# Optimization experiments

Hardware: AMD Instinct MI355X
Metric: run time of the kernel (lower is better)

The kernel has to match this reference:

```python
import jax, jax.numpy as jnp
import numpy as np

EMBED_DIM = 1024
NUM_HEADS = 16
HEAD_DIM = EMBED_DIM // NUM_HEADS
BATCH = 4
SEQ = 2048


def setup_inputs() -> dict:
    key = jax.random.key(0)
    ks = jax.random.split(key, 9)
    s = 1.0 / np.sqrt(EMBED_DIM)
    return {
        "query": jax.random.normal(ks[0], (BATCH, SEQ, EMBED_DIM), jnp.float32),
        "Wq": jax.random.normal(ks[1], (EMBED_DIM, EMBED_DIM), jnp.float32) * s,
        "bq": jnp.zeros((EMBED_DIM,), jnp.float32),
        "Wk": jax.random.normal(ks[2], (EMBED_DIM, EMBED_DIM), jnp.float32) * s,
        "bk": jnp.zeros((EMBED_DIM,), jnp.float32),
        "Wv": jax.random.normal(ks[3], (EMBED_DIM, EMBED_DIM), jnp.float32) * s,
        "bv": jnp.zeros((EMBED_DIM,), jnp.float32),
        "Wo": jax.random.normal(ks[4], (EMBED_DIM, EMBED_DIM), jnp.float32) * s,
        "bo": jnp.zeros((EMBED_DIM,), jnp.float32),
    }


def reference(query, Wq, bq, Wk, bk, Wv, bv, Wo, bo):
    bsz, seq, embed_dim = query.shape
    scaling = HEAD_DIM ** (-0.5)
    # projections (torch Linear: x @ W.T + b)
    q = (query @ Wq.T + bq) * scaling
    k = query @ Wk.T + bk
    v = query @ Wv.T + bv
    # [b, h, s, d]
    q = q.reshape(bsz, seq, NUM_HEADS, HEAD_DIM).transpose(0, 2, 1, 3)
    k = k.reshape(bsz, seq, NUM_HEADS, HEAD_DIM).transpose(0, 2, 1, 3)
    v = v.reshape(bsz, seq, NUM_HEADS, HEAD_DIM).transpose(0, 2, 1, 3)
    # full [b, h, s, s] scores (faithful to the naive original)
    scores = jnp.einsum("bhqd,bhkd->bhqk", q, k)
    causal = jnp.tril(jnp.ones((seq, seq), bool))  # [s, s]
    scores = jnp.where(causal[None, None], scores, -jnp.inf)
    probs = jax.nn.softmax(scores, axis=-1)
    attn = jnp.einsum("bhqk,bhkd->bhqd", probs, v)
    attn = attn.transpose(0, 2, 1, 3).reshape(bsz, seq, embed_dim)
    return attn @ Wo.T + bo
```

## Files before the change

kernel.cpp:

```cpp
#include <hip/hip_runtime.h>
#include <stdint.h>

typedef unsigned short u16;
typedef __attribute__((ext_vector_type(8))) __bf16 bf16x8;
typedef __attribute__((ext_vector_type(4))) float f32x4;

#define SEQL 2048
#define NHEADS 16
#define HDIM 64
#define BSZ 4
#define EMB 1024
#define MROWS (BSZ * SEQL)
#define LOG2E 1.44269504088896f
#define NKT 32

__device__ __forceinline__ u16 f2bf(float f) {
  union { float f; uint32_t u; } v; v.f = f;
  return (u16)((v.u + 0x7fffu + ((v.u >> 16) & 1u)) >> 16);
}

__device__ __forceinline__ void g2l(const u16* g, u16* l) {
  __builtin_amdgcn_global_load_lds(
      (__attribute__((address_space(1))) void*)(g),
      (__attribute__((address_space(3))) void*)(l), 16, 0, 0);
}

__device__ __forceinline__ void cvt8(const float* __restrict__ in, u16* __restrict__ out, int i) {
  float4 a = *(const float4*)(in + i);
  float4 b = *(const float4*)(in + i + 4);
  uint4 o;
  o.x = f2bf(a.x) | ((uint32_t)f2bf(a.y) << 16);
  o.y = f2bf(a.z) | ((uint32_t)f2bf(a.w) << 16);
  o.z = f2bf(b.x) | ((uint32_t)f2bf(b.y) << 16);
  o.w = f2bf(b.z) | ((uint32_t)f2bf(b.w) << 16);
  *(uint4*)(out + i) = o;
}

#define XN (MROWS * EMB)
__global__ void cvt_all(const float* __restrict__ query,
                        const float* __restrict__ w0, const float* __restrict__ w1,
                        const float* __restrict__ w2, const float* __restrict__ w3,
                        u16* __restrict__ Xb, u16* __restrict__ Wqb) {
  int i = (blockIdx.x * blockDim.x + threadIdx.x) * 8;
  if (i < XN) {
    cvt8(query, Xb, i);
  } else {
    int j = i - XN;
    int w = j >> 20;
    int jj = j & 1048575;
    const float* src = w == 0 ? w0 : w == 1 ? w1 : w == 2 ? w2 : w3;
    cvt8(src, Wqb + ((size_t)w << 20), jj);
  }
}

#define GBODY3(WSTR, RBUF, DOPF, PFT, WBUF)                                         \
  {                                                                                 \
    asm volatile("s_waitcnt " WSTR ::: "memory");                                   \
    __builtin_amdgcn_sched_barrier(0);                                              \
    __builtin_amdgcn_s_barrier();                                                   \
    __builtin_amdgcn_sched_barrier(0);                                              \
    if (DOPF) {                                                                     \
      u16* d = lds + (WBUF) * 12288;                                                \
      g2l(Agb + (PFT) * 32, d + tid * 8);                                           \
      g2l(Bgb0 + (PFT) * 32, d + 4096 + tid * 8);                                   \
      g2l(Bgb1 + (PFT) * 32, d + 8192 + tid * 8);                                   \
    }                                                                               \
    const u16* Ab = lds + (RBUF) * 12288;                                           \
    const u16* Bb = Ab + 4096;                                                      \
    bf16x8 af[4], bfr[4];                                                           \
    _Pragma("unroll") for (int i = 0; i < 4; ++i) {                                 \
      af[i] = *(const bf16x8*)(Ab + (wr * 64 + i * 16 + lrow) * 32 + kg);           \
      bfr[i] = *(const bf16x8*)(Bb + (wc * 64 + i * 16 + lrow) * 32 + kg);          \
    }                                                                               \
    __builtin_amdgcn_s_setprio(1);                                                  \
    _Pragma("unroll") for (int mi = 0; mi < 4; ++mi)                                \
      _Pragma("unroll") for (int ni = 0; ni < 4; ++ni)                              \
        acc[mi][ni] =                                                               \
            __builtin_amdgcn_mfma_f32_16x16x32_bf16(af[mi], bfr[ni], acc[mi][ni],   \
                                                    0, 0, 0);                       \
    __builtin_amdgcn_s_setprio(0);                                                  \
  }

__device__ __forceinline__ void gemm_core256(const u16* __restrict__ A,
                                             const u16* __restrict__ B,
                                             int m0, int n0, u16* lds,
                                             f32x4 acc[4][4]) {
  const int tid = threadIdx.x;
  const int lane = tid & 63, wid = tid >> 6;
  const int wr = wid >> 2, wc = wid & 3;
  const int lrow = lane & 15, kg = (lane >> 4) * 8;
  const int srow = tid >> 2, scolE = (tid & 3) * 8;

  const u16* Agb  = A + (size_t)(m0 + srow) * EMB + scolE;
  const u16* Bgb0 = B + (size_t)(n0 + srow) * EMB + scolE;
  const u16* Bgb1 = B + (size_t)(n0 + 128 + srow) * EMB + scolE;

#pragma unroll
  for (int t = 0; t < 2; ++t) {
    u16* d = lds + t * 12288;
    g2l(Agb + t * 32, d + tid * 8);
    g2l(Bgb0 + t * 32, d + 4096 + tid * 8);
    g2l(Bgb1 + t * 32, d + 8192 + tid * 8);
  }

  int rb = 0;
#pragma unroll 1
  for (int kt = 0; kt < NKT - 2; ++kt) {
    int wb = rb + 2; if (wb >= 3) wb -= 3;
    GBODY3("vmcnt(3)", rb, true, kt + 2, wb)
    ++rb; if (rb == 3) rb = 0;
  }
  GBODY3("vmcnt(3)", rb, false, 0, 0)
  { int rb2 = rb + 1; if (rb2 == 3) rb2 = 0;
    GBODY3("vmcnt(0)", rb2, false, 0, 0) }
}

__global__ __launch_bounds__(512, 4) void gemm_qkv3(
    const u16* __restrict__ X, const u16* __restrict__ Wcat,
    const float* __restrict__ bq, const float* __restrict__ bk, const float* __restrict__ bv,
    u16* __restrict__ Qb, u16* __restrict__ Kb, u16* __restrict__ Vt) {
  __shared__ u16 lds[3 * 12288];
  const int orig = blockIdx.x;
  const int virt = (orig & 7) * 96 + (orig >> 3);
  const int mt = virt / 12, nt = virt % 12;

  const f32x4 fzero = {0.f, 0.f, 0.f, 0.f};
  f32x4 acc[4][4];
#pragma unroll
  for (int i = 0; i < 4; ++i)
#pragma unroll
    for (int j = 0; j < 4; ++j) acc[i][j] = fzero;

  gemm_core256(X, Wcat, mt * 128, nt * 256, lds, acc);

  const int tid = threadIdx.x, lane = tid & 63, wid = tid >> 6;
  const int wr = wid >> 2, wc = wid & 3;
  const int lrow = lane & 15, g = lane >> 4;
  const int which = nt >> 2;
  const float* bias = which == 0 ? bq : which == 1 ? bk : bv;
  const float scale = which == 0 ? 0.125f * LOG2E : 1.0f;

  if (which == 2) {
#pragma unroll
    for (int mi = 0; mi < 4; ++mi)
#pragma unroll
      for (int ni = 0; ni < 4; ++ni) {
        int n = nt * 256 + wc * 64 + ni * 16 + lrow;
        int nn = n & 1023;
        float bs = bias[nn];
        int h = nn >> 6, d = nn & 63;
        int m0r = mt * 128 + wr * 64 + mi * 16 + g * 4;
        int b = m0r >> 11, s = m0r & 2047;
        union { u16 s4[4]; uint2 u; } o;
#pragma unroll
        for (int r = 0; r < 4; ++r) o.s4[r] = f2bf(acc[mi][ni][r] + bs);
        *(uint2*)(Vt + ((size_t)(b * NHEADS + h) * HDIM + d) * SEQL + s) = o.u;
      }
  } else {
    u16* Ob = which == 0 ? Qb : Kb;
#pragma unroll
    for (int mi = 0; mi < 4; ++mi)
#pragma unroll
      for (int ni = 0; ni < 4; ++ni) {
        int n = nt * 256 + wc * 64 + ni * 16 + lrow;
        int nn = n & 1023;
        float bs = bias[nn];
        int h = nn >> 6, d = nn & 63;
#pragma unroll
        for (int r = 0; r < 4; ++r) {
          int m = mt * 128 + wr * 64 + mi * 16 + g * 4 + r;
          int b = m >> 11, s = m & 2047;
          float v = (acc[mi][ni][r] + bs) * scale;
          Ob[(size_t)((b * NHEADS + h) * SEQL + s) * HDIM + d] = f2bf(v);
        }
      }
  }
}

__global__ __launch_bounds__(512, 4) void gemm_out2(
    const u16* __restrict__ Ain, const u16* __restrict__ Wo,
    const float* __restrict__ bo, float* __restrict__ out) {
  __shared__ u16 lds[3 * 12288];
  const int orig = blockIdx.x;
  const int virt = (orig & 7) * 32 + (orig >> 3);
  const int mt = virt >> 2, nt = virt & 3;

  const f32x4 fzero = {0.f, 0.f, 0.f, 0.f};
  f32x4 acc[4][4];
#pragma unroll
  for (int i = 0; i < 4; ++i)
#pragma unroll
    for (int j = 0; j < 4; ++j) acc[i][j] = fzero;

  gemm_core256(Ain, Wo, mt * 128, nt * 256, lds, acc);

  const int tid = threadIdx.x, lane = tid & 63, wid = tid >> 6;
  const int wr = wid >> 2, wc = wid & 3;
  const int lrow = lane & 15, g = lane >> 4;
#pragma unroll
  for (int mi = 0; mi < 4; ++mi)
#pragma unroll
    for (int ni = 0; ni < 4; ++ni) {
      int n = nt * 256 + wc * 64 + ni * 16 + lrow;
      float bs = bo[n];
#pragma unroll
      for (int r = 0; r < 4; ++r) {
        int m = mt * 128 + wr * 64 + mi * 16 + g * 4 + r;
        out[(size_t)m * EMB + n] = acc[mi][ni][r] + bs;
      }
    }
}

__device__ __forceinline__ int swz(int row, int colE) {
  return row * 64 + (colE ^ ((row & 7) << 3));
}

__global__ __launch_bounds__(256, 4) void attn4_kernel(
    const u16* __restrict__ Qb, const u16* __restrict__ Kb, const u16* __restrict__ Vt,
    u16* __restrict__ Ab) {
  __shared__ u16 Ks[2][64 * 64];
  __shared__ u16 Vs[2][64 * 64];

  const int bid = blockIdx.x;
  const int qa  = bid >> 6;
  const int bh  = bid & 63;

  const int tid = threadIdx.x, lane = tid & 63, wid = tid >> 6;
  const int lrow = lane & 15, g = lane >> 4, kg = g * 8;

  const u16* Qbh = Qb + (size_t)bh * SEQL * HDIM;
  const u16* Kbh = Kb + (size_t)bh * SEQL * HDIM;
  const u16* Vbh = Vt + (size_t)bh * HDIM * SEQL;

  const int srow = tid >> 3;
  const int sce  = (tid & 7) * 8;

  const f32x4 fzero = {0.f, 0.f, 0.f, 0.f};
  const int b = bh >> 4, h = bh & 15;

#pragma unroll 1
  for (int ph = 0; ph < 2; ++ph) {
    const int qt = ph ? (31 - qa) : qa;
    const int q0 = qt * 64;
    const int NT = qt + 1;

    const int qrow = q0 + wid * 16 + lrow;
    const bf16x8 qf0 = *(const bf16x8*)(Qbh + (size_t)qrow * HDIM + kg);
    const bf16x8 qf1 = *(const bf16x8*)(Qbh + (size_t)qrow * HDIM + 32 + kg);

    float m_run = -1e30f, l_run = 0.f;
    f32x4 accO[4];
#pragma unroll
    for (int d = 0; d < 4; ++d) accO[d] = fzero;

    {
      uint4 k0 = *(const uint4*)(Kbh + (size_t)srow * HDIM + sce);
      uint4 k1 = *(const uint4*)(Kbh + (size_t)(srow + 32) * HDIM + sce);
      uint4 v0 = *(const uint4*)(Vbh + (size_t)srow * SEQL + sce);
      uint4 v1 = *(const uint4*)(Vbh + (size_t)(srow + 32) * SEQL + sce);
      *(uint4*)(&Ks[0][swz(srow, sce)]) = k0;
      *(uint4*)(&Ks[0][swz(srow + 32, sce)]) = k1;
      *(uint4*)(&Vs[0][swz(srow, sce)]) = v0;
      *(uint4*)(&Vs[0][swz(srow + 32, sce)]) = v1;
    }
    __syncthreads();

    for (int t = 0; t < NT; ++t) {
      const int cur = t & 1;
      const int kv0 = t * 64;
      const bool pf = (t + 1 < NT);
      uint4 k0, k1, v0, v1;
      if (pf) {
        const int kvn = kv0 + 64;
        k0 = *(const uint4*)(Kbh + (size_t)(kvn + srow) * HDIM + sce);
        k1 = *(const uint4*)(Kbh + (size_t)(kvn + srow + 32) * HDIM + sce);
        v0 = *(const uint4*)(Vbh + (size_t)srow * SEQL + kvn + sce);
        v1 = *(const uint4*)(Vbh + (size_t)(srow + 32) * SEQL + kvn + sce);
      }

      f32x4 sacc[4];
      __builtin_amdgcn_s_setprio(1);
#pragma unroll
      for (int kb = 0; kb < 4; ++kb) {
        bf16x8 kfa = *(const bf16x8*)(&Ks[cur][swz(kb * 16 + lrow, kg)]);
        bf16x8 kfb = *(const bf16x8*)(&Ks[cur][swz(kb * 16 + lrow, 32 + kg)]);
        f32x4 z = fzero;
        z = __builtin_amdgcn_mfma_f32_16x16x32_bf16(kfa, qf0, z, 0, 0, 0);
        z = __builtin_amdgcn_mfma_f32_16x16x32_bf16(kfb, qf1, z, 0, 0, 0);
        sacc[kb] = z;
      }
      __builtin_amdgcn_s_setprio(0);

      if (kv0 + 63 > q0 + wid * 16) {
#pragma unroll
        for (int kb = 0; kb < 4; ++kb)
#pragma unroll
          for (int r = 0; r < 4; ++r)
            if (kv0 + kb * 16 + g * 4 + r > qrow) sacc[kb][r] = -1e30f;
      }

      float mx = sacc[0][0];
#pragma unroll
      for (int kb = 0; kb < 4; ++kb)
#pragma unroll
        for (int r = 0; r < 4; ++r) mx = fmaxf(mx, sacc[kb][r]);
      mx = fmaxf(mx, __shfl_xor(mx, 16));
      mx = fmaxf(mx, __shfl_xor(mx, 32));

      if (!__all(mx <= m_run + 8.f)) {
        const float mnew = fmaxf(m_run, mx);
        const float sc = __builtin_amdgcn_exp2f(m_run - mnew);
        m_run = mnew;
        l_run *= sc;
#pragma unroll
        for (int d = 0; d < 4; ++d) accO[d] *= sc;
      }

      bf16x8 pa[2];
      float ls = 0.f;
#pragma unroll
      for (int kb = 0; kb < 4; ++kb)
#pragma unroll
        for (int r = 0; r < 4; ++r) {
          float p = __builtin_amdgcn_exp2f(sacc[kb][r] - m_run);
          ls += p;
          pa[kb >> 1][(kb & 1) * 4 + r] = (__bf16)p;
        }
      l_run += ls;

      __builtin_amdgcn_s_setprio(1);
#pragma unroll
      for (int ks = 0; ks < 2; ++ks)
#pragma unroll
        for (int d = 0; d < 4; ++d) {
          union { ushort4 h2[2]; bf16x8 v; } vf;
          vf.h2[0] = *(const ushort4*)(&Vs[cur][swz(d * 16 + lrow, ks * 32 + g * 4)]);
          vf.h2[1] = *(const ushort4*)(&Vs[cur][swz(d * 16 + lrow, ks * 32 + 16 + g * 4)]);
          accO[d] = __builtin_amdgcn_mfma_f32_16x16x32_bf16(vf.v, pa[ks], accO[d], 0, 0, 0);
        }
      __builtin_amdgcn_s_setprio(0);

      if (pf) {
        const int nb = cur ^ 1;
        *(uint4*)(&Ks[nb][swz(srow, sce)]) = k0;
        *(uint4*)(&Ks[nb][swz(srow + 32, sce)]) = k1;
        *(uint4*)(&Vs[nb][swz(srow, sce)]) = v0;
        *(uint4*)(&Vs[nb][swz(srow + 32, sce)]) = v1;
      }
      __syncthreads();
    }

    float l = l_run;
    l += __shfl_xor(l, 16);
    l += __shfl_xor(l, 32);
    const float inv = 1.f / l;
#pragma unroll
    for (int d = 0; d < 4; ++d) {
      union { u16 s4[4]; uint2 u; } o;
#pragma unroll
      for (int r = 0; r < 4; ++r) o.s4[r] = f2bf(accO[d][r] * inv);
      *(uint2*)(Ab + (size_t)(b * SEQL + qrow) * EMB + h * HDIM + d * 16 + g * 4) = o.u;
    }
    __syncthreads();
  }
}

extern "C" void kernel_launch(void* const* d_in, const int* in_sizes, int n_in,
                              void* d_out, int out_size, void* d_ws, size_t ws_size,
                              hipStream_t stream) {
  (void)in_sizes; (void)n_in; (void)out_size; (void)ws_size;
  const float* query = (const float*)d_in[0];
  const float* Wq = (const float*)d_in[1];
  const float* bq = (const float*)d_in[2];
  const float* Wk = (const float*)d_in[3];
  const float* bk = (const float*)d_in[4];
  const float* Wv = (const float*)d_in[5];
  const float* bv = (const float*)d_in[6];
  const float* Wo = (const float*)d_in[7];
  const float* bo = (const float*)d_in[8];
  float* out = (float*)d_out;

  const size_t MB = 1u << 20;
  char* ws = (char*)d_ws;
  u16* Xb  = (u16*)(ws);
  u16* Wqb = (u16*)(ws + 16 * MB);
  u16* Wob = (u16*)(ws + 22 * MB);
  u16* Qbf = (u16*)(ws + 24 * MB);
  u16* Kbf = (u16*)(ws + 40 * MB);
  u16* Vtg = (u16*)(ws + 56 * MB);
  u16* Ab  = Xb;

  cvt_all<<<6144, 256, 0, stream>>>(query, Wq, Wk, Wv, Wo, Xb, Wqb);
  gemm_qkv3<<<768, 512, 0, stream>>>(Xb, Wqb, bq, bk, bv, Qbf, Kbf, Vtg);
  attn4_kernel<<<1024, 256, 0, stream>>>(Qbf, Kbf, Vtg, Ab);
  gemm_out2<<<256, 512, 0, stream>>>(Ab, Wob, bo, out);
}
```

Before: 160.1 us.

## Shrink GEMM tiles to 128x128 with 4-wave blocks; tree-reduce softmax max/sum

Both projection GEMMs move from 128x256 tiles on 8-wave blocks to 128x128 tiles on 4-wave blocks. That doubles the grid (1536 and 512 blocks) and cuts LDS per stage, with matching changes to the staging loads, vmcnt counts, swizzled block mapping and epilogue indexing. The aim is better occupancy and tail balance, especially for the output GEMM, which previously had only 256 blocks. The cost is less operand reuse per block and more global and L2 traffic. The attention kernel also switches its row max and exp-sum to tree reductions to shorten serial dependency chains.

```diff
diff --git a/kernel.cpp b/kernel.cpp
--- a/kernel.cpp
+++ b/kernel.cpp
@@ -53,19 +53,20 @@
   }
 }
 
-#define GBODY3(WSTR, RBUF, DOPF, PFT, WBUF)                                         \
+#define GBODY2(WSTR, RBUF, DOPF, PFT, WBUF)                                         \
   {                                                                                 \
     asm volatile("s_waitcnt " WSTR ::: "memory");                                   \
     __builtin_amdgcn_sched_barrier(0);                                              \
     __builtin_amdgcn_s_barrier();                                                   \
     __builtin_amdgcn_sched_barrier(0);                                              \
     if (DOPF) {                                                                     \
-      u16* d = lds + (WBUF) * 12288;                                                \
+      u16* d = lds + (WBUF) * 8192;                                                 \
       g2l(Agb + (PFT) * 32, d + tid * 8);                                           \
-      g2l(Bgb0 + (PFT) * 32, d + 4096 + tid * 8);                                   \
-      g2l(Bgb1 + (PFT) * 32, d + 8192 + tid * 8);                                   \
+      g2l(Agb + (PFT) * 32 + 64 * EMB, d + 2048 + tid * 8);                         \
+      g2l(Bgb + (PFT) * 32, d + 4096 + tid * 8);                                    \
+      g2l(Bgb + (PFT) * 32 + 64 * EMB, d + 6144 + tid * 8);                         \
     }                                                                               \
-    const u16* Ab = lds + (RBUF) * 12288;                                           \
+    const u16* Ab = lds + (RBUF) * 8192;                                            \
     const u16* Bb = Ab + 4096;                                                      \
     bf16x8 af[4], bfr[4];                                                           \
     _Pragma("unroll") for (int i = 0; i < 4; ++i) {                                 \
@@ -81,48 +82,48 @@
     __builtin_amdgcn_s_setprio(0);                                                  \
   }
 
-__device__ __forceinline__ void gemm_core256(const u16* __restrict__ A,
+__device__ __forceinline__ void gemm_core128(const u16* __restrict__ A,
                                              const u16* __restrict__ B,
                                              int m0, int n0, u16* lds,
                                              f32x4 acc[4][4]) {
   const int tid = threadIdx.x;
   const int lane = tid & 63, wid = tid >> 6;
-  const int wr = wid >> 2, wc = wid & 3;
+  const int wr = wid >> 1, wc = wid & 1;
   const int lrow = lane & 15, kg = (lane >> 4) * 8;
   const int srow = tid >> 2, scolE = (tid & 3) * 8;
 
-  const u16* Agb  = A + (size_t)(m0 + srow) * EMB + scolE;
-  const u16* Bgb0 = B + (size_t)(n0 + srow) * EMB + scolE;
-  const u16* Bgb1 = B + (size_t)(n0 + 128 + srow) * EMB + scolE;
+  const u16* Agb = A + (size_t)(m0 + srow) * EMB + scolE;
+  const u16* Bgb = B + (size_t)(n0 + srow) * EMB + scolE;
 
 #pragma unroll
   for (int t = 0; t < 2; ++t) {
-    u16* d = lds + t * 12288;
+    u16* d = lds + t * 8192;
     g2l(Agb + t * 32, d + tid * 8);
-    g2l(Bgb0 + t * 32, d + 4096 + tid * 8);
-    g2l(Bgb1 + t * 32, d + 8192 + tid * 8);
+    g2l(Agb + t * 32 + 64 * EMB, d + 2048 + tid * 8);
+    g2l(Bgb + t * 32, d + 4096 + tid * 8);
+    g2l(Bgb + t * 32 + 64 * EMB, d + 6144 + tid * 8);
   }
 
   int rb = 0;
 #pragma unroll 1
   for (int kt = 0; kt < NKT - 2; ++kt) {
     int wb = rb + 2; if (wb >= 3) wb -= 3;
-    GBODY3("vmcnt(3)", rb, true, kt + 2, wb)
+    GBODY2("vmcnt(4)", rb, true, kt + 2, wb)
     ++rb; if (rb == 3) rb = 0;
   }
-  GBODY3("vmcnt(3)", rb, false, 0, 0)
+  GBODY2("vmcnt(4)", rb, false, 0, 0)
   { int rb2 = rb + 1; if (rb2 == 3) rb2 = 0;
-    GBODY3("vmcnt(0)", rb2, false, 0, 0) }
-}
-
-__global__ __launch_bounds__(512, 4) void gemm_qkv3(
+    GBODY2("vmcnt(0)", rb2, false, 0, 0) }
+}
+
+__global__ __launch_bounds__(256, 3) void gemm_qkv3(
     const u16* __restrict__ X, const u16* __restrict__ Wcat,
     const float* __restrict__ bq, const float* __restrict__ bk, const float* __restrict__ bv,
     u16* __restrict__ Qb, u16* __restrict__ Kb, u16* __restrict__ Vt) {
-  __shared__ u16 lds[3 * 12288];
+  __shared__ u16 lds[3 * 8192];
   const int orig = blockIdx.x;
-  const int virt = (orig & 7) * 96 + (orig >> 3);
-  const int mt = virt / 12, nt = virt % 12;
+  const int virt = (orig & 7) * 192 + (orig >> 3);
+  const int mt = virt / 24, nt = virt % 24;
 
   const f32x4 fzero = {0.f, 0.f, 0.f, 0.f};
   f32x4 acc[4][4];
@@ -131,12 +132,12 @@
 #pragma unroll
     for (int j = 0; j < 4; ++j) acc[i][j] = fzero;
 
-  gemm_core256(X, Wcat, mt * 128, nt * 256, lds, acc);
+  gemm_core128(X, Wcat, mt * 128, nt * 128, lds, acc);
 
   const int tid = threadIdx.x, lane = tid & 63, wid = tid >> 6;
-  const int wr = wid >> 2, wc = wid & 3;
+  const int wr = wid >> 1, wc = wid & 1;
   const int lrow = lane & 15, g = lane >> 4;
-  const int which = nt >> 2;
+  const int which = nt >> 3;
   const float* bias = which == 0 ? bq : which == 1 ? bk : bv;
   const float scale = which == 0 ? 0.125f * LOG2E : 1.0f;
 
@@ -145,7 +146,7 @@
     for (int mi = 0; mi < 4; ++mi)
 #pragma unroll
       for (int ni = 0; ni < 4; ++ni) {
-        int n = nt * 256 + wc * 64 + ni * 16 + lrow;
+        int n = nt * 128 + wc * 64 + ni * 16 + lrow;
         int nn = n & 1023;
         float bs = bias[nn];
         int h = nn >> 6, d = nn & 63;
@@ -162,7 +163,7 @@
     for (int mi = 0; mi < 4; ++mi)
 #pragma unroll
       for (int ni = 0; ni < 4; ++ni) {
-        int n = nt * 256 + wc * 64 + ni * 16 + lrow;
+        int n = nt * 128 + wc * 64 + ni * 16 + lrow;
         int nn = n & 1023;
         float bs = bias[nn];
         int h = nn >> 6, d = nn & 63;
@@ -177,13 +178,13 @@
   }
 }
 
-__global__ __launch_bounds__(512, 4) void gemm_out2(
+__global__ __launch_bounds__(256, 3) void gemm_out2(
     const u16* __restrict__ Ain, const u16* __restrict__ Wo,
     const float* __restrict__ bo, float* __restrict__ out) {
-  __shared__ u16 lds[3 * 12288];
+  __shared__ u16 lds[3 * 8192];
   const int orig = blockIdx.x;
-  const int virt = (orig & 7) * 32 + (orig >> 3);
-  const int mt = virt >> 2, nt = virt & 3;
+  const int virt = (orig & 7) * 64 + (orig >> 3);
+  const int mt = virt >> 3, nt = virt & 7;
 
   const f32x4 fzero = {0.f, 0.f, 0.f, 0.f};
   f32x4 acc[4][4];
@@ -192,16 +193,16 @@
 #pragma unroll
     for (int j = 0; j < 4; ++j) acc[i][j] = fzero;
 
-  gemm_core256(Ain, Wo, mt * 128, nt * 256, lds, acc);
+  gemm_core128(Ain, Wo, mt * 128, nt * 128, lds, acc);
 
   const int tid = threadIdx.x, lane = tid & 63, wid = tid >> 6;
-  const int wr = wid >> 2, wc = wid & 3;
+  const int wr = wid >> 1, wc = wid & 1;
   const int lrow = lane & 15, g = lane >> 4;
 #pragma unroll
   for (int mi = 0; mi < 4; ++mi)
 #pragma unroll
     for (int ni = 0; ni < 4; ++ni) {
-      int n = nt * 256 + wc * 64 + ni * 16 + lrow;
+      int n = nt * 128 + wc * 64 + ni * 16 + lrow;
       float bs = bo[n];
 #pragma unroll
       for (int r = 0; r < 4; ++r) {
@@ -299,11 +300,11 @@
             if (kv0 + kb * 16 + g * 4 + r > qrow) sacc[kb][r] = -1e30f;
       }
 
-      float mx = sacc[0][0];
-#pragma unroll
-      for (int kb = 0; kb < 4; ++kb)
-#pragma unroll
-        for (int r = 0; r < 4; ++r) mx = fmaxf(mx, sacc[kb][r]);
+      float t0 = fmaxf(fmaxf(sacc[0][0], sacc[0][1]), fmaxf(sacc[0][2], sacc[0][3]));
+      float t1 = fmaxf(fmaxf(sacc[1][0], sacc[1][1]), fmaxf(sacc[1][2], sacc[1][3]));
+      float t2 = fmaxf(fmaxf(sacc[2][0], sacc[2][1]), fmaxf(sacc[2][2], sacc[2][3]));
+      float t3 = fmaxf(fmaxf(sacc[3][0], sacc[3][1]), fmaxf(sacc[3][2], sacc[3][3]));
+      float mx = fmaxf(fmaxf(t0, t1), fmaxf(t2, t3));
       mx = fmaxf(mx, __shfl_xor(mx, 16));
       mx = fmaxf(mx, __shfl_xor(mx, 32));
 
@@ -317,16 +318,20 @@
       }
 
       bf16x8 pa[2];
-      float ls = 0.f;
-#pragma unroll
-      for (int kb = 0; kb < 4; ++kb)
-#pragma unroll
-        for (int r = 0; r < 4; ++r) {
-          float p = __builtin_amdgcn_exp2f(sacc[kb][r] - m_run);
-          ls += p;
-          pa[kb >> 1][(kb & 1) * 4 + r] = (__bf16)p;
-        }
-      l_run += ls;
+      float lp[4];
+#pragma unroll
+      for (int kb = 0; kb < 4; ++kb) {
+        float p0 = __builtin_amdgcn_exp2f(sacc[kb][0] - m_run);
+        float p1 = __builtin_amdgcn_exp2f(sacc[kb][1] - m_run);
+        float p2 = __builtin_amdgcn_exp2f(sacc[kb][2] - m_run);
+        float p3 = __builtin_amdgcn_exp2f(sacc[kb][3] - m_run);
+        lp[kb] = (p0 + p1) + (p2 + p3);
+        pa[kb >> 1][(kb & 1) * 4 + 0] = (__bf16)p0;
+        pa[kb >> 1][(kb & 1) * 4 + 1] = (__bf16)p1;
+        pa[kb >> 1][(kb & 1) * 4 + 2] = (__bf16)p2;
+        pa[kb >> 1][(kb & 1) * 4 + 3] = (__bf16)p3;
+      }
+      l_run += (lp[0] + lp[1]) + (lp[2] + lp[3]);
 
       __builtin_amdgcn_s_setprio(1);
 #pragma unroll
@@ -391,7 +396,7 @@
   u16* Ab  = Xb;
 
   cvt_all<<<6144, 256, 0, stream>>>(query, Wq, Wk, Wv, Wo, Xb, Wqb);
-  gemm_qkv3<<<768, 512, 0, stream>>>(Xb, Wqb, bq, bk, bv, Qbf, Kbf, Vtg);
+  gemm_qkv3<<<1536, 256, 0, stream>>>(Xb, Wqb, bq, bk, bv, Qbf, Kbf, Vtg);
   attn4_kernel<<<1024, 256, 0, stream>>>(Qbf, Kbf, Vtg, Ab);
-  gemm_out2<<<256, 512, 0, stream>>>(Ab, Wob, bo, out);
-}
+  gemm_out2<<<512, 256, 0, stream>>>(Ab, Wob, bo, out);
+}
```

After: 168.9 us. +5.5%, slower.

## Software-pipeline attention: compute next tile's QK scores during current softmax/PV

Applied to the files above, without the earlier changes.

Restructures the attention inner loop so the QK^T MFMAs for tile t+1 are issued in the same iteration as the softmax and PV of tile t. K gets a triple-buffered LDS ring and is prefetched two tiles ahead, while V stays double-buffered one tile ahead. This is meant to let MFMA work overlap the exp/max VALU work and hide LDS latency. In exchange it uses more LDS and registers (sa/sb score sets), which may reduce occupancy, and the loop is now kept rolled with unroll 1.

```diff
diff --git a/kernel.cpp b/kernel.cpp
--- a/kernel.cpp
+++ b/kernel.cpp
@@ -215,10 +215,10 @@
   return row * 64 + (colE ^ ((row & 7) << 3));
 }
 
-__global__ __launch_bounds__(256, 4) void attn4_kernel(
+__global__ __launch_bounds__(256, 4) void attn5_kernel(
     const u16* __restrict__ Qb, const u16* __restrict__ Kb, const u16* __restrict__ Vt,
     u16* __restrict__ Ab) {
-  __shared__ u16 Ks[2][64 * 64];
+  __shared__ u16 Ks[3][64 * 64];
   __shared__ u16 Vs[2][64 * 64];
 
   const int bid = blockIdx.x;
@@ -262,48 +262,80 @@
       *(uint4*)(&Ks[0][swz(srow + 32, sce)]) = k1;
       *(uint4*)(&Vs[0][swz(srow, sce)]) = v0;
       *(uint4*)(&Vs[0][swz(srow + 32, sce)]) = v1;
+      if (NT > 1) {
+        uint4 k2 = *(const uint4*)(Kbh + (size_t)(64 + srow) * HDIM + sce);
+        uint4 k3 = *(const uint4*)(Kbh + (size_t)(64 + srow + 32) * HDIM + sce);
+        *(uint4*)(&Ks[1][swz(srow, sce)]) = k2;
+        *(uint4*)(&Ks[1][swz(srow + 32, sce)]) = k3;
+      }
     }
     __syncthreads();
 
+    f32x4 sa[4];
+    __builtin_amdgcn_s_setprio(1);
+#pragma unroll
+    for (int kb = 0; kb < 4; ++kb) {
+      bf16x8 kfa = *(const bf16x8*)(&Ks[0][swz(kb * 16 + lrow, kg)]);
+      bf16x8 kfb = *(const bf16x8*)(&Ks[0][swz(kb * 16 + lrow, 32 + kg)]);
+      f32x4 z = fzero;
+      z = __builtin_amdgcn_mfma_f32_16x16x32_bf16(kfa, qf0, z, 0, 0, 0);
+      z = __builtin_amdgcn_mfma_f32_16x16x32_bf16(kfb, qf1, z, 0, 0, 0);
+      sa[kb] = z;
+    }
+    __builtin_amdgcn_s_setprio(0);
+    if (63 > q0 + wid * 16) {
+#pragma unroll
+      for (int kb = 0; kb < 4; ++kb)
+#pragma unroll
+        for (int r = 0; r < 4; ++r)
+          if (kb * 16 + g * 4 + r > qrow) sa[kb][r] = -1e30f;
+    }
+
+    int kB1 = 1, kB2 = 2;
+#pragma unroll 1
     for (int t = 0; t < NT; ++t) {
-      const int cur = t & 1;
-      const int kv0 = t * 64;
-      const bool pf = (t + 1 < NT);
-      uint4 k0, k1, v0, v1;
-      if (pf) {
-        const int kvn = kv0 + 64;
-        k0 = *(const uint4*)(Kbh + (size_t)(kvn + srow) * HDIM + sce);
-        k1 = *(const uint4*)(Kbh + (size_t)(kvn + srow + 32) * HDIM + sce);
-        v0 = *(const uint4*)(Vbh + (size_t)srow * SEQL + kvn + sce);
-        v1 = *(const uint4*)(Vbh + (size_t)(srow + 32) * SEQL + kvn + sce);
-      }
-
-      f32x4 sacc[4];
-      __builtin_amdgcn_s_setprio(1);
-#pragma unroll
-      for (int kb = 0; kb < 4; ++kb) {
-        bf16x8 kfa = *(const bf16x8*)(&Ks[cur][swz(kb * 16 + lrow, kg)]);
-        bf16x8 kfb = *(const bf16x8*)(&Ks[cur][swz(kb * 16 + lrow, 32 + kg)]);
-        f32x4 z = fzero;
-        z = __builtin_amdgcn_mfma_f32_16x16x32_bf16(kfa, qf0, z, 0, 0, 0);
-        z = __builtin_amdgcn_mfma_f32_16x16x32_bf16(kfb, qf1, z, 0, 0, 0);
-        sacc[kb] = z;
-      }
-      __builtin_amdgcn_s_setprio(0);
-
-      if (kv0 + 63 > q0 + wid * 16) {
-#pragma unroll
-        for (int kb = 0; kb < 4; ++kb)
-#pragma unroll
-          for (int r = 0; r < 4; ++r)
-            if (kv0 + kb * 16 + g * 4 + r > qrow) sacc[kb][r] = -1e30f;
-      }
-
-      float mx = sacc[0][0];
+      const bool hasN1 = (t + 1 < NT);
+      const bool hasN2 = (t + 2 < NT);
+      uint4 pk0, pk1, pv0, pv1;
+      if (hasN2) {
+        const int kvn = (t + 2) * 64;
+        pk0 = *(const uint4*)(Kbh + (size_t)(kvn + srow) * HDIM + sce);
+        pk1 = *(const uint4*)(Kbh + (size_t)(kvn + srow + 32) * HDIM + sce);
+      }
+      if (hasN1) {
+        const int kvn = (t + 1) * 64;
+        pv0 = *(const uint4*)(Vbh + (size_t)srow * SEQL + kvn + sce);
+        pv1 = *(const uint4*)(Vbh + (size_t)(srow + 32) * SEQL + kvn + sce);
+      }
+
+      f32x4 sb[4];
+      if (hasN1) {
+        __builtin_amdgcn_s_setprio(1);
+#pragma unroll
+        for (int kb = 0; kb < 4; ++kb) {
+          bf16x8 kfa = *(const bf16x8*)(&Ks[kB1][swz(kb * 16 + lrow, kg)]);
+          bf16x8 kfb = *(const bf16x8*)(&Ks[kB1][swz(kb * 16 + lrow, 32 + kg)]);
+          f32x4 z = fzero;
+          z = __builtin_amdgcn_mfma_f32_16x16x32_bf16(kfa, qf0, z, 0, 0, 0);
+          z = __builtin_amdgcn_mfma_f32_16x16x32_bf16(kfb, qf1, z, 0, 0, 0);
+          sb[kb] = z;
+        }
+        __builtin_amdgcn_s_setprio(0);
+        const int kv0n = (t + 1) * 64;
+        if (kv0n + 63 > q0 + wid * 16) {
+#pragma unroll
+          for (int kb = 0; kb < 4; ++kb)
+#pragma unroll
+            for (int r = 0; r < 4; ++r)
+              if (kv0n + kb * 16 + g * 4 + r > qrow) sb[kb][r] = -1e30f;
+        }
+      }
+
+      float mx = sa[0][0];
 #pragma unroll
       for (int kb = 0; kb < 4; ++kb)
 #pragma unroll
-        for (int r = 0; r < 4; ++r) mx = fmaxf(mx, sacc[kb][r]);
+        for (int r = 0; r < 4; ++r) mx = fmaxf(mx, sa[kb][r]);
       mx = fmaxf(mx, __shfl_xor(mx, 16));
       mx = fmaxf(mx, __shfl_xor(mx, 32));
 
@@ -322,7 +354,7 @@
       for (int kb = 0; kb < 4; ++kb)
 #pragma unroll
         for (int r = 0; r < 4; ++r) {
-          float p = __builtin_amdgcn_exp2f(sacc[kb][r] - m_run);
+          float p = __builtin_amdgcn_exp2f(sa[kb][r] - m_run);
           ls += p;
           pa[kb >> 1][(kb & 1) * 4 + r] = (__bf16)p;
         }
@@ -334,20 +366,25 @@
 #pragma unroll
         for (int d = 0; d < 4; ++d) {
           union { ushort4 h2[2]; bf16x8 v; } vf;
-          vf.h2[0] = *(const ushort4*)(&Vs[cur][swz(d * 16 + lrow, ks * 32 + g * 4)]);
-          vf.h2[1] = *(const ushort4*)(&Vs[cur][swz(d * 16 + lrow, ks * 32 + 16 + g * 4)]);
+          vf.h2[0] = *(const ushort4*)(&Vs[t & 1][swz(d * 16 + lrow, ks * 32 + g * 4)]);
+          vf.h2[1] = *(const ushort4*)(&Vs[t & 1][swz(d * 16 + lrow, ks * 32 + 16 + g * 4)]);
           accO[d] = __builtin_amdgcn_mfma_f32_16x16x32_bf16(vf.v, pa[ks], accO[d], 0, 0, 0);
         }
       __builtin_amdgcn_s_setprio(0);
 
-      if (pf) {
-        const int nb = cur ^ 1;
-        *(uint4*)(&Ks[nb][swz(srow, sce)]) = k0;
-        *(uint4*)(&Ks[nb][swz(srow + 32, sce)]) = k1;
-        *(uint4*)(&Vs[nb][swz(srow, sce)]) = v0;
-        *(uint4*)(&Vs[nb][swz(srow + 32, sce)]) = v1;
+      if (hasN2) {
+        *(uint4*)(&Ks[kB2][swz(srow, sce)]) = pk0;
+        *(uint4*)(&Ks[kB2][swz(srow + 32, sce)]) = pk1;
+      }
+      if (hasN1) {
+        *(uint4*)(&Vs[(t + 1) & 1][swz(srow, sce)]) = pv0;
+        *(uint4*)(&Vs[(t + 1) & 1][swz(srow + 32, sce)]) = pv1;
       }
       __syncthreads();
+
+      if (hasN1) { sa[0] = sb[0]; sa[1] = sb[1]; sa[2] = sb[2]; sa[3] = sb[3]; }
+      ++kB1; if (kB1 == 3) kB1 = 0;
+      ++kB2; if (kB2 == 3) kB2 = 0;
     }
 
     float l = l_run;
@@ -392,6 +429,6 @@
 
   cvt_all<<<6144, 256, 0, stream>>>(query, Wq, Wk, Wv, Wo, Xb, Wqb);
   gemm_qkv3<<<768, 512, 0, stream>>>(Xb, Wqb, bq, bk, bv, Qbf, Kbf, Vtg);
-  attn4_kernel<<<1024, 256, 0, stream>>>(Qbf, Kbf, Vtg, Ab);
+  attn5_kernel<<<1024, 256, 0, stream>>>(Qbf, Kbf, Vtg, Ab);
   gemm_out2<<<256, 512, 0, stream>>>(Ab, Wob, bo, out);
 }
```

After: 186.2 us. 1.16x slower.
